# Optimization experiments

Measured on AMD Instinct MI355X. Metric: run time of the kernel, lower is better.

The kernel has to match this reference:

```python
import jax, jax.numpy as jnp
import numpy as np

DIM = 192
HEADS = 8
EPS = 1e-12  # torch F.normalize eps


def _l2norm(t):
    # normalize over last axis, matching torch.nn.functional.normalize
    n = jnp.sqrt(jnp.sum(t * t, axis=-1, keepdims=True))
    return t / jnp.maximum(n, EPS)


def setup_inputs() -> dict:
    key = jax.random.key(0)
    k1, k2, k3, k4 = jax.random.split(key, 4)
    B, C, H, W = 16, DIM, 128, 128
    s = 1.0 / np.sqrt(C)
    return {
        "x": jax.random.normal(k1, (B, C, H, W), dtype=jnp.float32),
        "w_qkv": jax.random.normal(k2, (C, 3 * C), dtype=jnp.float32) * s,
        "w_proj": jax.random.normal(k3, (C, C), dtype=jnp.float32) * s,
        "b_proj": jax.random.normal(k4, (C,), dtype=jnp.float32) * 0.01,
        "temperature": jnp.ones((HEADS, 1, 1), dtype=jnp.float32),
    }


def reference(x, w_qkv, w_proj, b_proj, temperature):
    B, C, H, W = x.shape
    N = H * W
    h = HEADS
    d = C // h
    # [B,C,H,W] -> [B,N,C]
    xt = x.reshape(B, C, N).transpose(0, 2, 1)
    qkv = (xt @ w_qkv).reshape(B, N, 3, h, d)
    qkv = qkv.transpose(2, 0, 3, 1, 4)           # [3,B,h,N,d]
    q, k, v = qkv[0], qkv[1], qkv[2]
    # transpose to channel-as-token: [B,h,d,N]
    q = _l2norm(q.transpose(0, 1, 3, 2))
    k = _l2norm(k.transpose(0, 1, 3, 2))
    v = v.transpose(0, 1, 3, 2)
    # small channel attention matrix [B,h,d,d]
    attn = jnp.einsum("bhdn,bhen->bhde", q, k) * temperature
    attn = jax.nn.softmax(attn, axis=-1)
    out = jnp.einsum("bhde,bhen->bhdn", attn, v)  # [B,h,d,N]
    out = out.transpose(0, 3, 1, 2).reshape(B, N, C)
    out = out @ w_proj + b_proj
    return out.transpose(0, 2, 1).reshape(B, C, H, W)
```

## Files before the change

### kernel.cpp

```cpp
#include <hip/hip_runtime.h>
#include <hip/hip_bf16.h>
#include <math.h>

#define C_DIM 192
#define NTOK 16384
#define NB 16
#define NH 8
#define HD 24
#define EPSN 1e-12f

typedef float f32x4 __attribute__((ext_vector_type(4)));
typedef __bf16 bf16x4 __attribute__((ext_vector_type(4)));
typedef __bf16 bf16x8 __attribute__((ext_vector_type(8)));

__device__ __forceinline__ f32x4 mfma16(bf16x8 a, bf16x8 b, f32x4 c) {
  return __builtin_amdgcn_mfma_f32_16x16x32_bf16(a, b, c, 0, 0, 0);
}

__device__ __forceinline__ bf16x8 cvt8(const float* __restrict__ p) {
  f32x4 a = *(const f32x4*)p;
  f32x4 b = *(const f32x4*)(p + 4);
  bf16x8 r;
  r[0] = (__bf16)a[0]; r[1] = (__bf16)a[1]; r[2] = (__bf16)a[2]; r[3] = (__bf16)a[3];
  r[4] = (__bf16)b[0]; r[5] = (__bf16)b[1]; r[6] = (__bf16)b[2]; r[7] = (__bf16)b[3];
  return r;
}

__global__ __launch_bounds__(256, 2) void k1_gram(const float* __restrict__ x,
                                                  float* __restrict__ gpart,
                                                  int kc) {
  const int b = blockIdx.y, chunk = blockIdx.x;
  const float* xb = x + (size_t)b * C_DIM * NTOK + (size_t)chunk * kc;
  __shared__ __bf16 xsh[2][C_DIM * 40];
  const int t = threadIdx.x;
  const int lane = t & 63, wid = t >> 6;
  const int lrow = lane & 15, loct = lane >> 4;
  const int r0 = (wid >> 1) * 96, c0 = (wid & 1) * 96;
  f32x4 acc[6][6] = {};
  f32x4 stg[6];

#pragma unroll
  for (int it = 0; it < 6; ++it) {
    int idx = it * 256 + t, r = idx >> 3, c8 = idx & 7;
    stg[it] = *(const f32x4*)(xb + (size_t)r * NTOK + 4 * c8);
  }
#pragma unroll
  for (int it = 0; it < 6; ++it) {
    int idx = it * 256 + t, r = idx >> 3, c8 = idx & 7;
    bf16x4 w;
    w[0] = (__bf16)stg[it][0]; w[1] = (__bf16)stg[it][1];
    w[2] = (__bf16)stg[it][2]; w[3] = (__bf16)stg[it][3];
    *(bf16x4*)(&xsh[0][r * 40 + 4 * c8]) = w;
  }
  __syncthreads();

  for (int ks = 0; ks < kc; ks += 32) {
    const int cur = (ks >> 5) & 1;
    const bool more = (ks + 32) < kc;
    if (more) {
#pragma unroll
      for (int it = 0; it < 6; ++it) {
        int idx = it * 256 + t, r = idx >> 3, c8 = idx & 7;
        stg[it] = *(const f32x4*)(xb + (size_t)r * NTOK + ks + 32 + 4 * c8);
      }
    }
    bf16x8 fa[6];
#pragma unroll
    for (int i = 0; i < 6; ++i)
      fa[i] = *(const bf16x8*)(&xsh[cur][(r0 + 16 * i + lrow) * 40 + 8 * loct]);
#pragma unroll
    for (int j = 0; j < 6; ++j) {
      bf16x8 fb = *(const bf16x8*)(&xsh[cur][(c0 + 16 * j + lrow) * 40 + 8 * loct]);
#pragma unroll
      for (int i = 0; i < 6; ++i) acc[i][j] = mfma16(fa[i], fb, acc[i][j]);
    }
    if (more) {
#pragma unroll
      for (int it = 0; it < 6; ++it) {
        int idx = it * 256 + t, r = idx >> 3, c8 = idx & 7;
        bf16x4 w;
        w[0] = (__bf16)stg[it][0]; w[1] = (__bf16)stg[it][1];
        w[2] = (__bf16)stg[it][2]; w[3] = (__bf16)stg[it][3];
        *(bf16x4*)(&xsh[cur ^ 1][r * 40 + 4 * c8]) = w;
      }
    }
    __syncthreads();
  }
  float* gp = gpart + ((size_t)chunk * NB + b) * C_DIM * C_DIM;
#pragma unroll
  for (int i = 0; i < 6; ++i)
#pragma unroll
    for (int j = 0; j < 6; ++j)
#pragma unroll
      for (int e = 0; e < 4; ++e)
        gp[(size_t)(r0 + 16 * i + 4 * loct + e) * C_DIM + (c0 + 16 * j + lrow)] =
            acc[i][j][e];
}

__global__ __launch_bounds__(256) void k2a_reduce(const float* __restrict__ gpart,
                                                  float* __restrict__ G,
                                                  int nchunk) {
  const size_t total = (size_t)NB * C_DIM * C_DIM;
  size_t e0 = ((size_t)blockIdx.x * 256 + threadIdx.x) * 4;
  f32x4 s = {};
  for (int c = 0; c < nchunk; ++c) s += *(const f32x4*)(gpart + c * total + e0);
  *(f32x4*)(G + e0) = s;
}

__global__ __launch_bounds__(256) void k2b1_t(const float* __restrict__ G,
                                              const float* __restrict__ wqkv,
                                              float* __restrict__ Tt) {
  const int b = blockIdx.y, rb = blockIdx.x;
  const int lane = threadIdx.x & 63, wid = threadIdx.x >> 6;
  const int lrow = lane & 15, loct = lane >> 4;
  const float* Gb = G + (size_t)b * C_DIM * C_DIM;
  const int ddA = rb * 64 + wid * 16 + lrow;
  f32x4 acc[12] = {};
  for (int s = 0; s < 6; ++s) {
    bf16x8 fa;
#pragma unroll
    for (int e = 0; e < 8; ++e)
      fa[e] = (__bf16)wqkv[(size_t)(32 * s + 8 * loct + e) * 576 + ddA];
#pragma unroll
    for (int j = 0; j < 12; ++j) {
      bf16x8 fb = cvt8(Gb + (size_t)(16 * j + lrow) * C_DIM + 32 * s + 8 * loct);
      acc[j] = mfma16(fa, fb, acc[j]);
    }
  }
  float* To = Tt + (size_t)b * 384 * C_DIM;
#pragma unroll
  for (int j = 0; j < 12; ++j)
#pragma unroll
    for (int e = 0; e < 4; ++e)
      To[(size_t)(rb * 64 + wid * 16 + 4 * loct + e) * C_DIM + 16 * j + lrow] =
          acc[j][e];
}

__global__ __launch_bounds__(256) void k2b2_attn(const float* __restrict__ Tt,
                                                 const float* __restrict__ wqkv,
                                                 const float* __restrict__ temp,
                                                 float* __restrict__ Yt) {
  const int b = blockIdx.y, h = blockIdx.x;
  __shared__ float SL[32][33];
  __shared__ float qn2L[HD], kn2L[HD];
  const int t = threadIdx.x;
  const int lane = t & 63, wid = t >> 6;
  const int lrow = lane & 15, loct = lane >> 4;
  const float* Tb = Tt + (size_t)b * 384 * C_DIM;
  const int r = wid >> 1, j = wid & 1;
  f32x4 acc = {};
  for (int s = 0; s < 6; ++s) {
    bf16x8 fa = cvt8(Tb + (size_t)(h * HD + 16 * r + lrow) * C_DIM + 32 * s + 8 * loct);
    bf16x8 fb;
#pragma unroll
    for (int e = 0; e < 8; ++e)
      fb[e] = (__bf16)wqkv[(size_t)(32 * s + 8 * loct + e) * 576 + 192 + h * HD +
                           16 * j + lrow];
    acc = mfma16(fa, fb, acc);
  }
#pragma unroll
  for (int e = 0; e < 4; ++e) {
    int d = 16 * r + 4 * loct + e, ee = 16 * j + lrow;
    if (d < HD && ee < HD) SL[d][ee] = acc[e];
  }
  if (t < 48) {
    const int dd = (t < 24) ? t : t - 24;
    const int row = ((t < 24) ? 0 : 192) + h * HD + dd;
    float s = 0.f;
    for (int c = 0; c < C_DIM; ++c)
      s += Tb[(size_t)row * C_DIM + c] * wqkv[(size_t)c * 576 + row];
    if (t < 24) qn2L[dd] = s; else kn2L[dd] = s;
  }
  __syncthreads();
  if (t < HD) {
    const float tp = temp[h];
    float nq = fmaxf(sqrtf(fmaxf(qn2L[t], 0.f)), EPSN);
    float lg[HD];
    float m = -1e30f;
#pragma unroll
    for (int e = 0; e < HD; ++e) {
      float nk = fmaxf(sqrtf(fmaxf(kn2L[e], 0.f)), EPSN);
      lg[e] = SL[t][e] / (nq * nk) * tp;
      m = fmaxf(m, lg[e]);
    }
    float sum = 0.f;
#pragma unroll
    for (int e = 0; e < HD; ++e) { lg[e] = __expf(lg[e] - m); sum += lg[e]; }
    float inv = 1.f / sum;
#pragma unroll
    for (int e = 0; e < HD; ++e) SL[t][e] = lg[e] * inv;
  }
  __syncthreads();
  if (t < C_DIM) {
    float wv[HD];
#pragma unroll
    for (int e = 0; e < HD; ++e)
      wv[e] = wqkv[(size_t)t * 576 + 384 + h * HD + e];
    float* Yo = Yt + ((size_t)b * C_DIM + t) * C_DIM + h * HD;
#pragma unroll
    for (int d = 0; d < HD; ++d) {
      float y = 0.f;
#pragma unroll
      for (int e = 0; e < HD; ++e) y += SL[d][e] * wv[e];
      Yo[d] = y;
    }
  }
}

__global__ __launch_bounds__(256) void k2c_m(const float* __restrict__ wproj,
                                             const float* __restrict__ Yt,
                                             __bf16* __restrict__ M) {
  const int b = blockIdx.y, rb = blockIdx.x;
  const int lane = threadIdx.x & 63, wid = threadIdx.x >> 6;
  const int lrow = lane & 15, loct = lane >> 4;
  const float* Yb = Yt + (size_t)b * C_DIM * C_DIM;
  const int coA = rb * 64 + wid * 16 + lrow;
  f32x4 acc[12] = {};
  for (int s = 0; s < 6; ++s) {
    bf16x8 fa;
#pragma unroll
    for (int e = 0; e < 8; ++e)
      fa[e] = (__bf16)wproj[(size_t)(32 * s + 8 * loct + e) * C_DIM + coA];
#pragma unroll
    for (int j = 0; j < 12; ++j) {
      bf16x8 fb = cvt8(Yb + (size_t)(16 * j + lrow) * C_DIM + 32 * s + 8 * loct);
      acc[j] = mfma16(fa, fb, acc[j]);
    }
  }
  __bf16* Mo = M + (size_t)b * C_DIM * C_DIM;
#pragma unroll
  for (int j = 0; j < 12; ++j)
#pragma unroll
    for (int e = 0; e < 4; ++e)
      Mo[(size_t)(rb * 64 + wid * 16 + 4 * loct + e) * C_DIM + 16 * j + lrow] =
          (__bf16)acc[j][e];
}

__global__ __launch_bounds__(256, 3) void k3_out(const float* __restrict__ x,
                                                 const __bf16* __restrict__ M,
                                                 const float* __restrict__ bproj,
                                                 float* __restrict__ out) {
  const int nt = blockIdx.x, half = blockIdx.y, b = blockIdx.z;
  const int rbase = half * 96;
  __shared__ __bf16 Ml[96 * C_DIM];
  __shared__ float biasL[96];
  const int t = threadIdx.x;
  const int lane = t & 63, w = t >> 6;
  const int lrow = lane & 15, loct = lane >> 4;

  const __bf16* Mb = M + (size_t)b * C_DIM * C_DIM + (size_t)rbase * C_DIM;
  for (int i = t; i < 96 * 24; i += 256) {
    int row = i / 24, ch = i % 24;
    bf16x8 v = *(const bf16x8*)(Mb + row * C_DIM + ch * 8);
    *(bf16x8*)(Ml + row * C_DIM + ((ch ^ (row & 7)) * 8)) = v;
  }
  if (t < 96) biasL[t] = bproj[rbase + t];
  __syncthreads();

  const float* xb = x + (size_t)b * C_DIM * NTOK;
  float* ob = out + (size_t)b * C_DIM * NTOK;
  const int n0 = nt * 256 + w * 64;

  f32x4 acc[6][4] = {};
  f32x4 xs4[8];
#pragma unroll
  for (int e = 0; e < 8; ++e)
    xs4[e] = *(const f32x4*)(xb + (size_t)(8 * loct + e) * NTOK + n0 + 4 * lrow);

  for (int s = 0; s < 6; ++s) {
    bf16x8 fb[4];
#pragma unroll
    for (int nf = 0; nf < 4; ++nf)
#pragma unroll
      for (int e = 0; e < 8; ++e)
        fb[nf][e] = (__bf16)xs4[e][nf];
    if (s < 5) {
#pragma unroll
      for (int e = 0; e < 8; ++e)
        xs4[e] = *(const f32x4*)(xb + (size_t)(32 * (s + 1) + 8 * loct + e) * NTOK +
                                 n0 + 4 * lrow);
    }
#pragma unroll
    for (int tt = 0; tt < 6; ++tt) {
      int rowb = 16 * tt + lrow;
      bf16x8 fa = *(const bf16x8*)(Ml + rowb * C_DIM +
                                   (((4 * s + loct) ^ (rowb & 7)) * 8));
#pragma unroll
      for (int nf = 0; nf < 4; ++nf)
        acc[tt][nf] = mfma16(fa, fb[nf], acc[tt][nf]);
    }
  }

  __syncthreads();
  float* epi_w = (float*)Ml + w * 1088;
#pragma unroll
  for (int tt = 0; tt < 6; ++tt) {
    f32x4 bias4 = *(const f32x4*)(biasL + 16 * tt + 4 * loct);
#pragma unroll
    for (int e = 0; e < 4; ++e) {
      f32x4 v;
      v[0] = acc[tt][0][e] + bias4[e];
      v[1] = acc[tt][1][e] + bias4[e];
      v[2] = acc[tt][2][e] + bias4[e];
      v[3] = acc[tt][3][e] + bias4[e];
      *(f32x4*)(epi_w + (4 * loct + e) * 68 + 4 * lrow) = v;
    }
#pragma unroll
    for (int h = 0; h < 4; ++h) {
      int r = 4 * h + loct;
      f32x4 v = *(const f32x4*)(epi_w + r * 68 + 4 * lrow);
      *(f32x4*)(ob + (size_t)(rbase + 16 * tt + r) * NTOK + n0 + 4 * lrow) = v;
    }
  }
}

extern "C" void kernel_launch(void* const* d_in, const int* in_sizes, int n_in,
                              void* d_out, int out_size, void* d_ws, size_t ws_size,
                              hipStream_t stream) {
  const float* x = (const float*)d_in[0];
  const float* wqkv = (const float*)d_in[1];
  const float* wproj = (const float*)d_in[2];
  const float* bproj = (const float*)d_in[3];
  const float* temp = (const float*)d_in[4];
  float* out = (float*)d_out;

  const size_t GSZ = (size_t)NB * C_DIM * C_DIM;
  const size_t TSZ = (size_t)NB * 384 * C_DIM;
  int nchunk = 32;
  while (nchunk > 1 &&
         ((size_t)nchunk * GSZ + GSZ + TSZ + GSZ + GSZ) * 4 > ws_size)
    nchunk >>= 1;
  float* wsf = (float*)d_ws;
  float* gpart = wsf;
  float* G = gpart + (size_t)nchunk * GSZ;
  float* Tt = G + GSZ;
  float* Yt = Tt + TSZ;
  __bf16* M = (__bf16*)(Yt + GSZ);

  k1_gram<<<dim3(nchunk, NB), 256, 0, stream>>>(x, gpart, NTOK / nchunk);
  k2a_reduce<<<dim3(576), 256, 0, stream>>>(gpart, G, nchunk);
  k2b1_t<<<dim3(6, NB), 256, 0, stream>>>(G, wqkv, Tt);
  k2b2_attn<<<dim3(NH, NB), 256, 0, stream>>>(Tt, wqkv, temp, Yt);
  k2c_m<<<dim3(3, NB), 256, 0, stream>>>(wproj, Yt, M);
  k3_out<<<dim3(NTOK / 256, 2, NB), 256, 0, stream>>>(x, M, bproj, out);
}
```

Baseline: 227.3 us.

## Load wide 256-token tiles into swizzled LDS for Gram kernel

```diff
diff --git a/kernel.cpp b/kernel.cpp
--- a/kernel.cpp
+++ b/kernel.cpp
@@ -26,66 +26,58 @@
   return r;
 }
 
-__global__ __launch_bounds__(256, 2) void k1_gram(const float* __restrict__ x,
-                                                  float* __restrict__ gpart,
-                                                  int kc) {
+__global__ __launch_bounds__(256) void k1_gram(const float* __restrict__ x,
+                                               float* __restrict__ gpart,
+                                               int kc) {
   const int b = blockIdx.y, chunk = blockIdx.x;
   const float* xb = x + (size_t)b * C_DIM * NTOK + (size_t)chunk * kc;
-  __shared__ __bf16 xsh[2][C_DIM * 40];
+  __shared__ __bf16 xs[C_DIM * 256];
   const int t = threadIdx.x;
   const int lane = t & 63, wid = t >> 6;
   const int lrow = lane & 15, loct = lane >> 4;
   const int r0 = (wid >> 1) * 96, c0 = (wid & 1) * 96;
   f32x4 acc[6][6] = {};
-  f32x4 stg[6];
-
-#pragma unroll
-  for (int it = 0; it < 6; ++it) {
-    int idx = it * 256 + t, r = idx >> 3, c8 = idx & 7;
-    stg[it] = *(const f32x4*)(xb + (size_t)r * NTOK + 4 * c8);
-  }
-#pragma unroll
-  for (int it = 0; it < 6; ++it) {
-    int idx = it * 256 + t, r = idx >> 3, c8 = idx & 7;
-    bf16x4 w;
-    w[0] = (__bf16)stg[it][0]; w[1] = (__bf16)stg[it][1];
-    w[2] = (__bf16)stg[it][2]; w[3] = (__bf16)stg[it][3];
-    *(bf16x4*)(&xsh[0][r * 40 + 4 * c8]) = w;
-  }
-  __syncthreads();
-
-  for (int ks = 0; ks < kc; ks += 32) {
-    const int cur = (ks >> 5) & 1;
-    const bool more = (ks + 32) < kc;
-    if (more) {
-#pragma unroll
-      for (int it = 0; it < 6; ++it) {
-        int idx = it * 256 + t, r = idx >> 3, c8 = idx & 7;
-        stg[it] = *(const f32x4*)(xb + (size_t)r * NTOK + ks + 32 + 4 * c8);
+
+  for (int ts = 0; ts < kc; ts += 256) {
+    const int rbase = wid * 48;
+#pragma unroll 1
+    for (int rb = 0; rb < 48; rb += 12) {
+      f32x4 v[12];
+#pragma unroll
+      for (int i = 0; i < 12; ++i)
+        v[i] = *(const f32x4*)(xb + (size_t)(rbase + rb + i) * NTOK + ts + 4 * lane);
+#pragma unroll
+      for (int i = 0; i < 12; ++i) {
+        const int row = rbase + rb + i;
+        bf16x4 w;
+        w[0] = (__bf16)v[i][0]; w[1] = (__bf16)v[i][1];
+        w[2] = (__bf16)v[i][2]; w[3] = (__bf16)v[i][3];
+        const int q = lane >> 1, h = lane & 1;
+        *(bf16x4*)(&xs[row * 256 + ((q ^ (row & 7)) * 8) + h * 4]) = w;
       }
     }
-    bf16x8 fa[6];
-#pragma unroll
-    for (int i = 0; i < 6; ++i)
-      fa[i] = *(const bf16x8*)(&xsh[cur][(r0 + 16 * i + lrow) * 40 + 8 * loct]);
-#pragma unroll
-    for (int j = 0; j < 6; ++j) {
-      bf16x8 fb = *(const bf16x8*)(&xsh[cur][(c0 + 16 * j + lrow) * 40 + 8 * loct]);
-#pragma unroll
-      for (int i = 0; i < 6; ++i) acc[i][j] = mfma16(fa[i], fb, acc[i][j]);
-    }
-    if (more) {
-#pragma unroll
-      for (int it = 0; it < 6; ++it) {
-        int idx = it * 256 + t, r = idx >> 3, c8 = idx & 7;
-        bf16x4 w;
-        w[0] = (__bf16)stg[it][0]; w[1] = (__bf16)stg[it][1];
-        w[2] = (__bf16)stg[it][2]; w[3] = (__bf16)stg[it][3];
-        *(bf16x4*)(&xsh[cur ^ 1][r * 40 + 4 * c8]) = w;
+    __syncthreads();
+#pragma unroll
+    for (int kk = 0; kk < 8; ++kk) {
+      bf16x8 fa[6];
+#pragma unroll
+      for (int i = 0; i < 6; ++i) {
+        const int row = r0 + 16 * i + lrow;
+        fa[i] = *(const bf16x8*)(&xs[row * 256 +
+                                     (((4 * kk + loct) ^ (row & 7)) * 8)]);
       }
+#pragma unroll
+      for (int j = 0; j < 6; ++j) {
+        const int row = c0 + 16 * j + lrow;
+        bf16x8 fb = *(const bf16x8*)(&xs[row * 256 +
+                                         (((4 * kk + loct) ^ (row & 7)) * 8)]);
+#pragma unroll
+        for (int i = 0; i < 6; ++i) acc[i][j] = mfma16(fa[i], fb, acc[i][j]);
+      }
     }
     __syncthreads();
   }
+
   float* gp = gpart + ((size_t)chunk * NB + b) * C_DIM * C_DIM;
 #pragma unroll
   for (int i = 0; i < 6; ++i)
```

After: 232.7 us. 1.02x slower.
